# Kernel optimization log

Hardware: AMD Instinct MI355X
Metric: run time of the kernel (lower is better)

Reference implementation:

```python
import jax, jax.numpy as jnp
import numpy as np

# Module hyperparameters (init_kwargs)
THRESHOLD_ABS = 0.2
THRESHOLD_REL = 0.05   # set to None to disable the relative-threshold branch
MIN_DISTANCE = 3


def setup_inputs() -> dict:
    key = jax.random.key(0)
    # belief maps in [0, 1), NCHW
    belive_map = jax.random.uniform(key, (32, 4, 512, 512), dtype=jnp.float32)
    return {"belive_map": belive_map}


def reference(belive_map):
    """Peak detection on belief maps (dense, jit-friendly form).

    Faithful to BeliveMapsNMS.forward: the torch module additionally compacts
    the mask into (coords, labels, scores) lists via nonzero/gather, which has
    data-dependent shapes; here we return the equivalent dense outputs:
      mask        [B,C,H,W] bool   - peak locations (nonzero of this == torch ind)
      scores_abs  [B,C,H,W] f32    - belief value at peaks, 0 elsewhere
      scores_rel  [B,C,H,W] f32    - scores_abs / per-(b,c) max
    """
    k = 2 * MIN_DISTANCE + 1          # 7
    pad = k // 2                       # 3 -> 'same' max pool, stride 1

    # F.max_pool2d(kernel=k, stride=1, padding=k//2)
    x_max = jax.lax.reduce_window(
        belive_map, -jnp.inf, jax.lax.max,
        window_dimensions=(1, 1, k, k),
        window_strides=(1, 1, 1, 1),
        padding=[(0, 0), (0, 0), (pad, pad), (pad, pad)],
    )

    # per-(batch, channel) global max: hh.max(dim=2) on the flattened map
    vmax = jnp.max(belive_map, axis=(2, 3), keepdims=True)  # [B,C,1,1]

    mask = (x_max == belive_map) & (belive_map > THRESHOLD_ABS)
    if THRESHOLD_REL is not None:
        mask = mask & (belive_map > THRESHOLD_REL * vmax)

    scores_abs = jnp.where(mask, belive_map, jnp.float32(0.0))
    scores_rel = scores_abs / vmax
    return mask, scores_abs, scores_rel
```

## Files before the change

kernel.cpp:

```cpp
#include <hip/hip_runtime.h>
#include <math.h>


#define H 512
#define W 512
#define PLANE_ELEMS (H * W)
#define TH 16
#define LROWS (TH + 6)
#define NEG_INF (-INFINITY)

typedef float v4f __attribute__((ext_vector_type(4)));

__device__ __forceinline__ float4 vmax4(float4 a, float4 b) {
    return make_float4(fmaxf(a.x, b.x), fmaxf(a.y, b.y), fmaxf(a.z, b.z), fmaxf(a.w, b.w));
}

__device__ __forceinline__ void nt_store4(float* p, float a, float b, float c, float d) {
    v4f v = {a, b, c, d};
    __builtin_nontemporal_store(v, (v4f*)p);
}

__global__ __launch_bounds__(256) void vmax_kernel(const float* __restrict__ in,
                                                   unsigned int* __restrict__ vmax_bits) {
    const int q = blockIdx.x;
    const int plane = blockIdx.y;
    const float4* p = (const float4*)(in + (size_t)plane * PLANE_ELEMS + q * (PLANE_ELEMS / 4));
    float m = 0.0f;
    const int nvec = PLANE_ELEMS / 4 / 4;
    for (int i = threadIdx.x; i < nvec; i += 256) {
        float4 v = p[i];
        m = fmaxf(m, fmaxf(fmaxf(v.x, v.y), fmaxf(v.z, v.w)));
    }
    #pragma unroll
    for (int o = 32; o > 0; o >>= 1) m = fmaxf(m, __shfl_down(m, o, 64));
    __shared__ float s[4];
    if ((threadIdx.x & 63) == 0) s[threadIdx.x >> 6] = m;
    __syncthreads();
    if (threadIdx.x == 0) {
        m = fmaxf(fmaxf(s[0], s[1]), fmaxf(s[2], s[3]));
        atomicMax(&vmax_bits[plane], __float_as_uint(m));
    }
}

__global__ __launch_bounds__(256) void nms_kernel(const float* __restrict__ in,
                                                  const unsigned int* __restrict__ vmax_bits,
                                                  float* __restrict__ out, int N) {
    const int plane = blockIdx.y;
    const int ty0 = blockIdx.x * TH;
    const float* pin = in + (size_t)plane * PLANE_ELEMS;

    __shared__ __align__(16) float sRow[LROWS * W];

    const int wid = threadIdx.x >> 6;
    const int lane = threadIdx.x & 63;
    const int c8 = lane << 3;

    for (int r = wid; r < LROWS; r += 4) {
        const int gy = ty0 + r - 3;
        float4 v0, v1;
        if (gy >= 0 && gy < H) {
            const float4* row = (const float4*)(pin + (size_t)gy * W);
            v0 = row[lane * 2];
            v1 = row[lane * 2 + 1];
        } else {
            v0 = v1 = make_float4(NEG_INF, NEG_INF, NEG_INF, NEG_INF);
        }
        float l0 = __shfl_up(v1.y, 1, 64), l1 = __shfl_up(v1.z, 1, 64), l2 = __shfl_up(v1.w, 1, 64);
        float r0 = __shfl_down(v0.x, 1, 64), r1 = __shfl_down(v0.y, 1, 64), r2 = __shfl_down(v0.z, 1, 64);
        if (lane == 0) { l0 = NEG_INF; l1 = NEG_INF; l2 = NEG_INF; }
        if (lane == 63) { r0 = NEG_INF; r1 = NEG_INF; r2 = NEG_INF; }
        float a[14] = {l0, l1, l2, v0.x, v0.y, v0.z, v0.w, v1.x, v1.y, v1.z, v1.w, r0, r1, r2};
        float A[7];
        A[6] = a[6];
        #pragma unroll
        for (int j = 5; j >= 0; --j) A[j] = fmaxf(a[j], A[j + 1]);
        float rm[8];
        rm[0] = A[0];
        float B = a[7];
        rm[1] = fmaxf(A[1], B);
        #pragma unroll
        for (int j = 2; j <= 6; ++j) { B = fmaxf(B, a[6 + j]); rm[j] = fmaxf(A[j], B); }
        B = fmaxf(B, a[13]);
        rm[7] = B;
        float4* dst = (float4*)&sRow[r * W + c8];
        dst[0] = make_float4(rm[0], rm[1], rm[2], rm[3]);
        dst[1] = make_float4(rm[4], rm[5], rm[6], rm[7]);
    }
    __syncthreads();

    const float vmax = __uint_as_float(vmax_bits[plane]);
    const float rel_thr = 0.05f * vmax;
    const float inv_vmax = 1.0f / vmax;

    float* __restrict__ omask = out;
    float* __restrict__ oabs = out + (size_t)N;
    float* __restrict__ orel = out + 2 * (size_t)N;

    const int strip = threadIdx.x >> 7;
    const int cg = threadIdx.x & 127;
    const int c = cg << 2;
    const int y0 = strip << 3;

    float4 Lr[7], Aq[7];
    #pragma unroll
    for (int k = 0; k < 7; ++k) Lr[k] = *(const float4*)&sRow[(y0 + k) * W + c];
    Aq[6] = Lr[6];
    #pragma unroll
    for (int j = 5; j >= 0; --j) Aq[j] = vmax4(Lr[j], Aq[j + 1]);

    const int gy_base = ty0 + y0;
    float4 Bq;
    #pragma unroll
    for (int i = 0; i < 8; ++i) {
        float4 m;
        if (i == 0) {
            m = Aq[0];
        } else {
            float4 row = *(const float4*)&sRow[(y0 + 6 + i) * W + c];
            Bq = (i == 1) ? row : vmax4(Bq, row);
            m = (i == 7) ? Bq : vmax4(Aq[i], Bq);
        }
        const int gy = gy_base + i;
        const float4 ctr = *(const float4*)(pin + (size_t)gy * W + c);
        const bool p0 = (m.x == ctr.x) & (ctr.x > 0.2f) & (ctr.x > rel_thr);
        const bool p1 = (m.y == ctr.y) & (ctr.y > 0.2f) & (ctr.y > rel_thr);
        const bool p2 = (m.z == ctr.z) & (ctr.z > 0.2f) & (ctr.z > rel_thr);
        const bool p3 = (m.w == ctr.w) & (ctr.w > 0.2f) & (ctr.w > rel_thr);
        const float a0 = p0 ? ctr.x : 0.0f, a1 = p1 ? ctr.y : 0.0f;
        const float a2 = p2 ? ctr.z : 0.0f, a3 = p3 ? ctr.w : 0.0f;
        const size_t o = (size_t)plane * PLANE_ELEMS + (size_t)gy * W + c;
        nt_store4(omask + o, p0 ? 1.0f : 0.0f, p1 ? 1.0f : 0.0f,
                             p2 ? 1.0f : 0.0f, p3 ? 1.0f : 0.0f);
        nt_store4(oabs + o, a0, a1, a2, a3);
        nt_store4(orel + o, a0 * inv_vmax, a1 * inv_vmax, a2 * inv_vmax, a3 * inv_vmax);
    }
}

extern "C" void kernel_launch(void* const* d_in, const int* in_sizes, int n_in,
                              void* d_out, int out_size, void* d_ws, size_t ws_size,
                              hipStream_t stream) {
    const float* in = (const float*)d_in[0];
    float* out = (float*)d_out;
    const int N = in_sizes[0];
    const int planes = N / PLANE_ELEMS;

    unsigned int* vmax_bits = (unsigned int*)d_ws;
    (void)hipMemsetAsync(vmax_bits, 0, planes * sizeof(unsigned int), stream);

    vmax_kernel<<<dim3(4, planes), 256, 0, stream>>>(in, vmax_bits);
    nms_kernel<<<dim3(H / TH, planes), 256, 0, stream>>>(in, vmax_bits, out, N);
}
```

Measured before the change: 492.9 us.

## Replace LDS tiling with per-wave register sliding window over row strips

The NMS kernel drops the shared-memory tile and barrier. Each wavefront now owns a 32-row strip of full-width rows and streams it with a register-resident sliding window: horizontal 7-max via lane shuffles, vertical 7-max via rolling prefix/suffix maxima over 4-row chunks, with the next rows prefetched. This cuts the halo overhead from 22/16 to 38/32 rows, removes the LDS round trip, and reads each centre value from registers instead of a second global load. In exchange each thread holds many live Row8 registers and the grid has fewer blocks (4 per plane), which may reduce occupancy and latency hiding.

```diff
diff --git a/kernel.cpp b/kernel.cpp
--- a/kernel.cpp
+++ b/kernel.cpp
@@ -5,19 +5,83 @@
 #define H 512
 #define W 512
 #define PLANE_ELEMS (H * W)
-#define TH 16
-#define LROWS (TH + 6)
+#define S 32
 #define NEG_INF (-INFINITY)
 
 typedef float v4f __attribute__((ext_vector_type(4)));
 
+struct Row8 { float4 lo, hi; };
+
 __device__ __forceinline__ float4 vmax4(float4 a, float4 b) {
     return make_float4(fmaxf(a.x, b.x), fmaxf(a.y, b.y), fmaxf(a.z, b.z), fmaxf(a.w, b.w));
+}
+__device__ __forceinline__ Row8 vmax8(Row8 a, Row8 b) {
+    Row8 r; r.lo = vmax4(a.lo, b.lo); r.hi = vmax4(a.hi, b.hi); return r;
 }
 
 __device__ __forceinline__ void nt_store4(float* p, float a, float b, float c, float d) {
     v4f v = {a, b, c, d};
     __builtin_nontemporal_store(v, (v4f*)p);
+}
+
+__device__ __forceinline__ Row8 loadRow(const float* __restrict__ pin, int gy, int lane) {
+    Row8 r;
+    if (gy >= 0 && gy < H) {
+        const float4* row = (const float4*)(pin + (size_t)gy * W);
+        r.lo = row[lane * 2];
+        r.hi = row[lane * 2 + 1];
+    } else {
+        r.lo = r.hi = make_float4(NEG_INF, NEG_INF, NEG_INF, NEG_INF);
+    }
+    return r;
+}
+
+__device__ __forceinline__ Row8 hmax7(Row8 v, int lane) {
+    float l0 = __shfl_up(v.hi.y, 1, 64), l1 = __shfl_up(v.hi.z, 1, 64), l2 = __shfl_up(v.hi.w, 1, 64);
+    float r0 = __shfl_down(v.lo.x, 1, 64), r1 = __shfl_down(v.lo.y, 1, 64), r2 = __shfl_down(v.lo.z, 1, 64);
+    if (lane == 0) { l0 = NEG_INF; l1 = NEG_INF; l2 = NEG_INF; }
+    if (lane == 63) { r0 = NEG_INF; r1 = NEG_INF; r2 = NEG_INF; }
+    float a[14] = {l0, l1, l2, v.lo.x, v.lo.y, v.lo.z, v.lo.w,
+                   v.hi.x, v.hi.y, v.hi.z, v.hi.w, r0, r1, r2};
+    float A[7];
+    A[6] = a[6];
+    #pragma unroll
+    for (int j = 5; j >= 0; --j) A[j] = fmaxf(a[j], A[j + 1]);
+    float rm[8];
+    rm[0] = A[0];
+    float B = a[7];
+    rm[1] = fmaxf(A[1], B);
+    #pragma unroll
+    for (int j = 2; j <= 6; ++j) { B = fmaxf(B, a[6 + j]); rm[j] = fmaxf(A[j], B); }
+    B = fmaxf(B, a[13]);
+    rm[7] = B;
+    Row8 out;
+    out.lo = make_float4(rm[0], rm[1], rm[2], rm[3]);
+    out.hi = make_float4(rm[4], rm[5], rm[6], rm[7]);
+    return out;
+}
+
+__device__ __forceinline__ void emitRow(float* __restrict__ om, float* __restrict__ oa,
+                                        float* __restrict__ orl, size_t off,
+                                        Row8 m, Row8 ctr, float rel_thr, float inv_vmax) {
+    const bool p0 = (m.lo.x == ctr.lo.x) & (ctr.lo.x > 0.2f) & (ctr.lo.x > rel_thr);
+    const bool p1 = (m.lo.y == ctr.lo.y) & (ctr.lo.y > 0.2f) & (ctr.lo.y > rel_thr);
+    const bool p2 = (m.lo.z == ctr.lo.z) & (ctr.lo.z > 0.2f) & (ctr.lo.z > rel_thr);
+    const bool p3 = (m.lo.w == ctr.lo.w) & (ctr.lo.w > 0.2f) & (ctr.lo.w > rel_thr);
+    const bool q0 = (m.hi.x == ctr.hi.x) & (ctr.hi.x > 0.2f) & (ctr.hi.x > rel_thr);
+    const bool q1 = (m.hi.y == ctr.hi.y) & (ctr.hi.y > 0.2f) & (ctr.hi.y > rel_thr);
+    const bool q2 = (m.hi.z == ctr.hi.z) & (ctr.hi.z > 0.2f) & (ctr.hi.z > rel_thr);
+    const bool q3 = (m.hi.w == ctr.hi.w) & (ctr.hi.w > 0.2f) & (ctr.hi.w > rel_thr);
+    const float a0 = p0 ? ctr.lo.x : 0.0f, a1 = p1 ? ctr.lo.y : 0.0f;
+    const float a2 = p2 ? ctr.lo.z : 0.0f, a3 = p3 ? ctr.lo.w : 0.0f;
+    const float b0 = q0 ? ctr.hi.x : 0.0f, b1 = q1 ? ctr.hi.y : 0.0f;
+    const float b2 = q2 ? ctr.hi.z : 0.0f, b3 = q3 ? ctr.hi.w : 0.0f;
+    nt_store4(om + off,     p0 ? 1.0f : 0.0f, p1 ? 1.0f : 0.0f, p2 ? 1.0f : 0.0f, p3 ? 1.0f : 0.0f);
+    nt_store4(om + off + 4, q0 ? 1.0f : 0.0f, q1 ? 1.0f : 0.0f, q2 ? 1.0f : 0.0f, q3 ? 1.0f : 0.0f);
+    nt_store4(oa + off,     a0, a1, a2, a3);
+    nt_store4(oa + off + 4, b0, b1, b2, b3);
+    nt_store4(orl + off,     a0 * inv_vmax, a1 * inv_vmax, a2 * inv_vmax, a3 * inv_vmax);
+    nt_store4(orl + off + 4, b0 * inv_vmax, b1 * inv_vmax, b2 * inv_vmax, b3 * inv_vmax);
 }
 
 __global__ __launch_bounds__(256) void vmax_kernel(const float* __restrict__ in,
@@ -42,97 +106,64 @@
     }
 }
 
-__global__ __launch_bounds__(256) void nms_kernel(const float* __restrict__ in,
-                                                  const unsigned int* __restrict__ vmax_bits,
-                                                  float* __restrict__ out, int N) {
+__global__ __launch_bounds__(256, 2) void nms_kernel(const float* __restrict__ in,
+                                                     const unsigned int* __restrict__ vmax_bits,
+                                                     float* __restrict__ out, int N) {
     const int plane = blockIdx.y;
-    const int ty0 = blockIdx.x * TH;
+    const int wid = threadIdx.x >> 6;
+    const int lane = threadIdx.x & 63;
+    const int r0 = (blockIdx.x * 4 + wid) * S;
     const float* pin = in + (size_t)plane * PLANE_ELEMS;
 
-    __shared__ __align__(16) float sRow[LROWS * W];
-
-    const int wid = threadIdx.x >> 6;
-    const int lane = threadIdx.x & 63;
-    const int c8 = lane << 3;
-
-    for (int r = wid; r < LROWS; r += 4) {
-        const int gy = ty0 + r - 3;
-        float4 v0, v1;
-        if (gy >= 0 && gy < H) {
-            const float4* row = (const float4*)(pin + (size_t)gy * W);
-            v0 = row[lane * 2];
-            v1 = row[lane * 2 + 1];
-        } else {
-            v0 = v1 = make_float4(NEG_INF, NEG_INF, NEG_INF, NEG_INF);
-        }
-        float l0 = __shfl_up(v1.y, 1, 64), l1 = __shfl_up(v1.z, 1, 64), l2 = __shfl_up(v1.w, 1, 64);
-        float r0 = __shfl_down(v0.x, 1, 64), r1 = __shfl_down(v0.y, 1, 64), r2 = __shfl_down(v0.z, 1, 64);
-        if (lane == 0) { l0 = NEG_INF; l1 = NEG_INF; l2 = NEG_INF; }
-        if (lane == 63) { r0 = NEG_INF; r1 = NEG_INF; r2 = NEG_INF; }
-        float a[14] = {l0, l1, l2, v0.x, v0.y, v0.z, v0.w, v1.x, v1.y, v1.z, v1.w, r0, r1, r2};
-        float A[7];
-        A[6] = a[6];
-        #pragma unroll
-        for (int j = 5; j >= 0; --j) A[j] = fmaxf(a[j], A[j + 1]);
-        float rm[8];
-        rm[0] = A[0];
-        float B = a[7];
-        rm[1] = fmaxf(A[1], B);
-        #pragma unroll
-        for (int j = 2; j <= 6; ++j) { B = fmaxf(B, a[6 + j]); rm[j] = fmaxf(A[j], B); }
-        B = fmaxf(B, a[13]);
-        rm[7] = B;
-        float4* dst = (float4*)&sRow[r * W + c8];
-        dst[0] = make_float4(rm[0], rm[1], rm[2], rm[3]);
-        dst[1] = make_float4(rm[4], rm[5], rm[6], rm[7]);
-    }
-    __syncthreads();
-
-    const float vmax = __uint_as_float(vmax_bits[plane]);
-    const float rel_thr = 0.05f * vmax;
-    const float inv_vmax = 1.0f / vmax;
+    const float vmaxv = __uint_as_float(vmax_bits[plane]);
+    const float rel_thr = 0.05f * vmaxv;
+    const float inv_vmax = 1.0f / vmaxv;
 
     float* __restrict__ omask = out;
     float* __restrict__ oabs = out + (size_t)N;
     float* __restrict__ orel = out + 2 * (size_t)N;
+    const size_t planeBase = (size_t)plane * PLANE_ELEMS;
+    const int c8 = lane << 3;
 
-    const int strip = threadIdx.x >> 7;
-    const int cg = threadIdx.x & 127;
-    const int c = cg << 2;
-    const int y0 = strip << 3;
+    Row8 hist[6], raw[3], fresh[4];
+    #pragma unroll
+    for (int j = 0; j < 6; ++j) {
+        Row8 rr = loadRow(pin, r0 - 3 + j, lane);
+        hist[j] = hmax7(rr, lane);
+        if (j >= 3) raw[j - 3] = rr;
+    }
+    #pragma unroll
+    for (int j = 0; j < 4; ++j) fresh[j] = loadRow(pin, r0 + 3 + j, lane);
 
-    float4 Lr[7], Aq[7];
     #pragma unroll
-    for (int k = 0; k < 7; ++k) Lr[k] = *(const float4*)&sRow[(y0 + k) * W + c];
-    Aq[6] = Lr[6];
-    #pragma unroll
-    for (int j = 5; j >= 0; --j) Aq[j] = vmax4(Lr[j], Aq[j + 1]);
-
-    const int gy_base = ty0 + y0;
-    float4 Bq;
-    #pragma unroll
-    for (int i = 0; i < 8; ++i) {
-        float4 m;
-        if (i == 0) {
-            m = Aq[0];
-        } else {
-            float4 row = *(const float4*)&sRow[(y0 + 6 + i) * W + c];
-            Bq = (i == 1) ? row : vmax4(Bq, row);
-            m = (i == 7) ? Bq : vmax4(Aq[i], Bq);
+    for (int k = 0; k < S / 4; ++k) {
+        const int R = r0 + 4 * k;
+        Row8 nxt[4];
+        if (k < S / 4 - 1) {
+            #pragma unroll
+            for (int j = 0; j < 4; ++j) nxt[j] = loadRow(pin, R + 7 + j, lane);
         }
-        const int gy = gy_base + i;
-        const float4 ctr = *(const float4*)(pin + (size_t)gy * W + c);
-        const bool p0 = (m.x == ctr.x) & (ctr.x > 0.2f) & (ctr.x > rel_thr);
-        const bool p1 = (m.y == ctr.y) & (ctr.y > 0.2f) & (ctr.y > rel_thr);
-        const bool p2 = (m.z == ctr.z) & (ctr.z > 0.2f) & (ctr.z > rel_thr);
-        const bool p3 = (m.w == ctr.w) & (ctr.w > 0.2f) & (ctr.w > rel_thr);
-        const float a0 = p0 ? ctr.x : 0.0f, a1 = p1 ? ctr.y : 0.0f;
-        const float a2 = p2 ? ctr.z : 0.0f, a3 = p3 ? ctr.w : 0.0f;
-        const size_t o = (size_t)plane * PLANE_ELEMS + (size_t)gy * W + c;
-        nt_store4(omask + o, p0 ? 1.0f : 0.0f, p1 ? 1.0f : 0.0f,
-                             p2 ? 1.0f : 0.0f, p3 ? 1.0f : 0.0f);
-        nt_store4(oabs + o, a0, a1, a2, a3);
-        nt_store4(orel + o, a0 * inv_vmax, a1 * inv_vmax, a2 * inv_vmax, a3 * inv_vmax);
+        Row8 hm[4];
+        #pragma unroll
+        for (int j = 0; j < 4; ++j) hm[j] = hmax7(fresh[j], lane);
+        Row8 sfx = vmax8(hist[4], hist[5]);
+        Row8 A3 = vmax8(hist[3], sfx);
+        Row8 A2 = vmax8(hist[2], A3);
+        Row8 A1 = vmax8(hist[1], A2);
+        Row8 A0 = vmax8(hist[0], A1);
+        Row8 B0 = hm[0];
+        Row8 B1 = vmax8(B0, hm[1]);
+        Row8 B2 = vmax8(B1, hm[2]);
+        Row8 B3 = vmax8(B2, hm[3]);
+        const size_t off = planeBase + (size_t)R * W + c8;
+        emitRow(omask, oabs, orel, off,         vmax8(A0, B0), raw[0],  rel_thr, inv_vmax);
+        emitRow(omask, oabs, orel, off + W,     vmax8(A1, B1), raw[1],  rel_thr, inv_vmax);
+        emitRow(omask, oabs, orel, off + 2 * W, vmax8(A2, B2), raw[2],  rel_thr, inv_vmax);
+        emitRow(omask, oabs, orel, off + 3 * W, vmax8(A3, B3), fresh[0], rel_thr, inv_vmax);
+        hist[0] = hist[4]; hist[1] = hist[5];
+        hist[2] = hm[0]; hist[3] = hm[1]; hist[4] = hm[2]; hist[5] = hm[3];
+        raw[0] = fresh[1]; raw[1] = fresh[2]; raw[2] = fresh[3];
+        fresh[0] = nxt[0]; fresh[1] = nxt[1]; fresh[2] = nxt[2]; fresh[3] = nxt[3];
     }
 }
 
@@ -148,5 +179,5 @@
     (void)hipMemsetAsync(vmax_bits, 0, planes * sizeof(unsigned int), stream);
 
     vmax_kernel<<<dim3(4, planes), 256, 0, stream>>>(in, vmax_bits);
-    nms_kernel<<<dim3(H / TH, planes), 256, 0, stream>>>(in, vmax_bits, out, N);
+    nms_kernel<<<dim3(H / (4 * S), planes), 256, 0, stream>>>(in, vmax_bits, out, N);
 }
```

Result: slower. 653.0 us (+32.5%).
